# Performance work log

Hardware: AMD Instinct MI355X
Metric: run time of the kernel (lower is better)

The kernel has to match this reference:

```python
import jax, jax.numpy as jnp
import numpy as np

FACTOR = 2.0
SCALE = 0.2
SOFTMAX_N = 0.0  # softmax_n param; n=0 -> standard softmax

B, H, S, D = 2, 16, 2048, 64


def setup_inputs() -> dict:
    key = jax.random.key(0)
    kq, kk, kv = jax.random.split(key, 3)
    return {
        "query": jax.random.normal(kq, (B, H, S, D), dtype=jnp.float32),
        "key": jax.random.normal(kk, (B, H, S, D), dtype=jnp.float32),
        "value": jax.random.normal(kv, (B, H, S, D), dtype=jnp.float32),
    }


def softmax_n(x, n):
    # exp(x) / (n + sum(exp(x))), numerically stable.
    m = jnp.max(x, axis=-1, keepdims=True)
    e = jnp.exp(x - m)
    denom = n * jnp.exp(-m) + jnp.sum(e, axis=-1, keepdims=True)
    return e / denom


def reference(query, key, value):
    # scores: [B,H,S,S]
    scores = jnp.einsum("bhqd,bhkd->bhqk", query, key) * SCALE
    attn = softmax_n(scores, SOFTMAX_N)
    out = jnp.einsum("bhqk,bhkd->bhqd", attn, value)
    return FACTOR * out
```

## Files before the change

### kernel.cpp

```cpp
#include <hip/hip_runtime.h>
#include <stdint.h>

typedef __attribute__((ext_vector_type(4))) float f32x4;
typedef __attribute__((ext_vector_type(8))) short s16x8;

__device__ __forceinline__ short f2bf(float f) {
    union { float f; uint32_t u; } v; v.f = f;
    uint32_t r = (v.u + 0x7FFFu + ((v.u >> 16) & 1u)) >> 16;
    return (short)(uint16_t)r;
}

__device__ __forceinline__ void async16(const short* g, short* lds) {
  __builtin_amdgcn_global_load_lds(
      (const __attribute__((address_space(1))) uint32_t*)g,
      (__attribute__((address_space(3))) uint32_t*)lds, 16, 0, 0);
}

__global__ __launch_bounds__(256) void conv_k_kernel(const float* __restrict__ K,
                                                     short* __restrict__ Kbf) {
  const int i = (blockIdx.x * 256 + threadIdx.x) * 8;
  f32x4 a = *(const f32x4*)(K + i);
  f32x4 b = *(const f32x4*)(K + i + 4);
  union { short s[8]; int4 v; } p;
#pragma unroll
  for (int j = 0; j < 4; ++j) { p.s[j] = f2bf(a[j]); p.s[4 + j] = f2bf(b[j]); }
  *(int4*)(Kbf + i) = p.v;
}

__global__ __launch_bounds__(256) void conv_vt_kernel(const float* __restrict__ V,
                                                      short* __restrict__ VT) {
  __shared__ short t[64][72];
  const int bh = blockIdx.x >> 5;
  const int st = blockIdx.x & 31;
  const size_t base = (size_t)bh * 131072;
  {
    const int s_loc = threadIdx.x >> 2;
    const int dch = (threadIdx.x & 3) * 16;
    const float* p = V + base + (size_t)(st * 64 + s_loc) * 64 + dch;
#pragma unroll
    for (int j = 0; j < 16; j += 4) {
      f32x4 a = *(const f32x4*)(p + j);
#pragma unroll
      for (int q = 0; q < 4; ++q) t[s_loc][dch + j + q] = f2bf(a[q]);
    }
  }
  __syncthreads();
  {
    const int d_loc = threadIdx.x >> 2;
    const int sch = (threadIdx.x & 3) * 16;
    union { short s[16]; int4 v[2]; } o;
#pragma unroll
    for (int j = 0; j < 16; ++j) o.s[j] = t[sch + j][d_loc];
    short* out = VT + base + (size_t)d_loc * 2048 + st * 64 + sch;
    *(int4*)(out) = o.v[0];
    *(int4*)(out + 8) = o.v[1];
  }
}

__global__ __launch_bounds__(256) void attn_fwd_v2(
    const float* __restrict__ Q, const short* __restrict__ Kbf,
    const short* __restrict__ VT, float* __restrict__ O) {
  constexpr int S = 2048, D = 64;
  constexpr float SCALE = 0.2f, FACTOR = 2.0f;
  constexpr int NT = S / 64;

  __shared__ short kT[2][4096];
  __shared__ short vT[2][4096];
  __shared__ short pT[4][1024];

  const int tid = threadIdx.x;
  const int w = tid >> 6;
  const int l = tid & 63;
  const int g = l >> 4;
  const int c = l & 15;

  const int rid = (blockIdx.x & 7) * 128 + (blockIdx.x >> 3);
  const int bh = rid >> 5;
  const int qt = rid & 31;
  const size_t base = (size_t)bh * (size_t)(S * D);

  const short* Kp = Kbf + base;
  const short* Vp = VT + base;
  char* pB = (char*)pT[w];

  s16x8 qa[2];
  {
    const float* qp = Q + base + (size_t)(qt * 64 + w * 16 + c) * D + g * 8;
#pragma unroll
    for (int kk = 0; kk < 2; ++kk) {
      f32x4 q0 = *(const f32x4*)(qp + kk * 32);
      f32x4 q1 = *(const f32x4*)(qp + kk * 32 + 4);
      s16x8 a;
#pragma unroll
      for (int i = 0; i < 4; ++i) { a[i] = f2bf(q0[i]); a[4 + i] = f2bf(q1[i]); }
      qa[kk] = a;
    }
  }

  int kOff[2], vOff[2], ldsT[2];
#pragma unroll
  for (int i = 0; i < 2; ++i) {
    const int t = i * 256 + w * 64 + l;
    const int row = t >> 3, ch = t & 7;
    ldsT[i] = t * 8;
    kOff[i] = row * 64 + ((ch ^ (row & 7)) << 3);
    vOff[i] = row * 2048 + ((ch ^ (row & 7)) << 3);
  }
#define STAGE(buf, kv0s)                                        \
  do {                                                          \
    _Pragma("unroll") for (int i = 0; i < 2; ++i) {             \
      async16(Kp + (kv0s) * 64 + kOff[i], &kT[buf][ldsT[i]]);   \
      async16(Vp + (kv0s) + vOff[i], &vT[buf][ldsT[i]]);        \
    }                                                           \
  } while (0)

  f32x4 o_acc[4];
#pragma unroll
  for (int nb = 0; nb < 4; ++nb) o_acc[nb] = (f32x4){0.f, 0.f, 0.f, 0.f};
  float m_r[4], l_r[4];
#pragma unroll
  for (int r = 0; r < 4; ++r) { m_r[r] = -1e30f; l_r[r] = 0.f; }

  int cur = 0;
  STAGE(0, 0);
  for (int kt = 0; kt < NT; ++kt) {
    __syncthreads();
    if (kt + 1 < NT) STAGE(cur ^ 1, (kt + 1) * 64);

    const char* kB = (const char*)kT[cur];
    const char* vB = (const char*)vT[cur];

    f32x4 sc[4];
#pragma unroll
    for (int nb = 0; nb < 4; ++nb) sc[nb] = (f32x4){0.f, 0.f, 0.f, 0.f};
#pragma unroll
    for (int kk = 0; kk < 2; ++kk) {
#pragma unroll
      for (int nb = 0; nb < 4; ++nb) {
        const int row = nb * 16 + c;
        s16x8 b = *(const s16x8*)(kB + row * 128 +
                                  ((kk * 64 + g * 16) ^ ((row & 7) << 4)));
        sc[nb] = __builtin_amdgcn_mfma_f32_16x16x32_bf16(qa[kk], b, sc[nb], 0, 0, 0);
      }
    }

    float p[4][4];
    float esc[4];
#pragma unroll
    for (int r = 0; r < 4; ++r) {
      float mx = fmaxf(fmaxf(sc[0][r], sc[1][r]), fmaxf(sc[2][r], sc[3][r]));
#pragma unroll
      for (int mask = 1; mask < 16; mask <<= 1)
        mx = fmaxf(mx, __shfl_xor(mx, mask, 64));
      mx *= SCALE;
      const float mnew = fmaxf(m_r[r], mx);
      esc[r] = __expf(m_r[r] - mnew);
      float rs = 0.f;
#pragma unroll
      for (int nb = 0; nb < 4; ++nb) {
        float e = __expf(sc[nb][r] * SCALE - mnew);
        p[nb][r] = e;
        rs += e;
      }
#pragma unroll
      for (int mask = 1; mask < 16; mask <<= 1)
        rs += __shfl_xor(rs, mask, 64);
      l_r[r] = l_r[r] * esc[r] + rs;
      m_r[r] = mnew;
    }
#pragma unroll
    for (int nb = 0; nb < 4; ++nb)
#pragma unroll
      for (int r = 0; r < 4; ++r)
        o_acc[nb][r] *= esc[r];

#pragma unroll
    for (int nb = 0; nb < 4; ++nb) {
#pragma unroll
      for (int r = 0; r < 4; ++r) {
        const int row = 4 * g + r;
        const int colb = (nb * 16 + c) * 2;
        *(short*)(pB + row * 128 + (colb ^ ((row & 7) << 4))) = f2bf(p[nb][r]);
      }
    }
    asm volatile("s_waitcnt lgkmcnt(0)" ::: "memory");

#pragma unroll
    for (int kk = 0; kk < 2; ++kk) {
      s16x8 pa = *(const s16x8*)(pB + c * 128 +
                                 ((kk * 64 + g * 16) ^ ((c & 7) << 4)));
#pragma unroll
      for (int nb = 0; nb < 4; ++nb) {
        const int row = nb * 16 + c;
        s16x8 vb = *(const s16x8*)(vB + row * 128 +
                                   ((kk * 64 + g * 16) ^ ((row & 7) << 4)));
        o_acc[nb] = __builtin_amdgcn_mfma_f32_16x16x32_bf16(pa, vb, o_acc[nb], 0, 0, 0);
      }
    }
    cur ^= 1;
  }
#undef STAGE

#pragma unroll
  for (int r = 0; r < 4; ++r) {
    const float f = FACTOR / l_r[r];
    const size_t rowg = (size_t)(qt * 64 + w * 16 + 4 * g + r);
    float* op = O + base + rowg * D + c;
#pragma unroll
    for (int nb = 0; nb < 4; ++nb) op[nb * 16] = o_acc[nb][r] * f;
  }
}

__global__ __launch_bounds__(256) void attn_fwd_v1(
    const float* __restrict__ Q, const float* __restrict__ K,
    const float* __restrict__ V, float* __restrict__ O) {
  constexpr int S = 2048, D = 64;
  constexpr float SCALE = 0.2f, FACTOR = 2.0f;
  constexpr int KVBLK = 64, NT = S / KVBLK;
  __shared__ short kT[64 * 64];
  __shared__ short vT[64 * 64];
  __shared__ short pT[4][16 * 64];
  const int tid = threadIdx.x;
  const int w = tid >> 6, l = tid & 63, g = l >> 4, c = l & 15;
  const int bh = blockIdx.x >> 5, qt = blockIdx.x & 31;
  const size_t base = (size_t)bh * (size_t)(S * D);
  char* kB = (char*)kT; char* vB = (char*)vT; char* pB = (char*)pT[w];
  s16x8 qa[2];
  {
    const float* qp = Q + base + (size_t)(qt * 64 + w * 16 + c) * D + g * 8;
#pragma unroll
    for (int kk = 0; kk < 2; ++kk) {
      f32x4 q0 = *(const f32x4*)(qp + kk * 32);
      f32x4 q1 = *(const f32x4*)(qp + kk * 32 + 4);
      s16x8 a;
#pragma unroll
      for (int i = 0; i < 4; ++i) { a[i] = f2bf(q0[i]); a[4 + i] = f2bf(q1[i]); }
      qa[kk] = a;
    }
  }
  f32x4 o_acc[4];
#pragma unroll
  for (int nb = 0; nb < 4; ++nb) o_acc[nb] = (f32x4){0.f, 0.f, 0.f, 0.f};
  float m_r[4], l_r[4];
#pragma unroll
  for (int r = 0; r < 4; ++r) { m_r[r] = -1e30f; l_r[r] = 0.f; }
  const int krow = tid >> 2, kcb = tid & 3;
  const int vpr = (tid >> 3) * 2, vpc = (tid & 7) * 8;
  for (int kt = 0; kt < NT; ++kt) {
    const int kv0 = kt * KVBLK;
    __syncthreads();
    {
      const float* kp = K + base + (size_t)(kv0 + krow) * D + kcb * 16;
      f32x4 a0 = *(const f32x4*)(kp);
      f32x4 a1 = *(const f32x4*)(kp + 4);
      f32x4 a2 = *(const f32x4*)(kp + 8);
      f32x4 a3 = *(const f32x4*)(kp + 12);
      union { short s[8]; int4 v; } p0, p1;
#pragma unroll
      for (int i = 0; i < 4; ++i) {
        p0.s[i] = f2bf(a0[i]); p0.s[4 + i] = f2bf(a1[i]);
        p1.s[i] = f2bf(a2[i]); p1.s[4 + i] = f2bf(a3[i]);
      }
      const int sw = (krow & 7) << 4;
      *(int4*)(kB + krow * 128 + ((kcb * 32) ^ sw)) = p0.v;
      *(int4*)(kB + krow * 128 + ((kcb * 32 + 16) ^ sw)) = p1.v;
    }
    {
      const float* vp = V + base + (size_t)(kv0 + vpr) * D + vpc;
      f32x4 r0a = *(const f32x4*)(vp);
      f32x4 r0b = *(const f32x4*)(vp + 4);
      f32x4 r1a = *(const f32x4*)(vp + D);
      f32x4 r1b = *(const f32x4*)(vp + D + 4);
      float lo[8] = {r0a[0], r0a[1], r0a[2], r0a[3], r0b[0], r0b[1], r0b[2], r0b[3]};
      float hi[8] = {r1a[0], r1a[1], r1a[2], r1a[3], r1b[0], r1b[1], r1b[2], r1b[3]};
#pragma unroll
      for (int i = 0; i < 8; ++i) {
        uint32_t pk = (uint32_t)(uint16_t)f2bf(lo[i]) |
                      ((uint32_t)(uint16_t)f2bf(hi[i]) << 16);
        const int col = vpc + i;
        *(uint32_t*)(vB + col * 128 + ((vpr * 2) ^ ((col & 7) << 4))) = pk;
      }
    }
    __syncthreads();
    f32x4 sc[4];
#pragma unroll
    for (int nb = 0; nb < 4; ++nb) sc[nb] = (f32x4){0.f, 0.f, 0.f, 0.f};
#pragma unroll
    for (int kk = 0; kk < 2; ++kk) {
#pragma unroll
      for (int nb = 0; nb < 4; ++nb) {
        const int row = nb * 16 + c;
        s16x8 b = *(const s16x8*)(kB + row * 128 +
                                  ((kk * 64 + g * 16) ^ ((row & 7) << 4)));
        sc[nb] = __builtin_amdgcn_mfma_f32_16x16x32_bf16(qa[kk], b, sc[nb], 0, 0, 0);
      }
    }
    float p[4][4]; float esc[4];
#pragma unroll
    for (int r = 0; r < 4; ++r) {
      float mx = fmaxf(fmaxf(sc[0][r], sc[1][r]), fmaxf(sc[2][r], sc[3][r]));
#pragma unroll
      for (int mask = 1; mask < 16; mask <<= 1)
        mx = fmaxf(mx, __shfl_xor(mx, mask, 64));
      mx *= SCALE;
      const float mnew = fmaxf(m_r[r], mx);
      esc[r] = __expf(m_r[r] - mnew);
      float rs = 0.f;
#pragma unroll
      for (int nb = 0; nb < 4; ++nb) {
        float e = __expf(sc[nb][r] * SCALE - mnew);
        p[nb][r] = e; rs += e;
      }
#pragma unroll
      for (int mask = 1; mask < 16; mask <<= 1)
        rs += __shfl_xor(rs, mask, 64);
      l_r[r] = l_r[r] * esc[r] + rs;
      m_r[r] = mnew;
    }
#pragma unroll
    for (int nb = 0; nb < 4; ++nb)
#pragma unroll
      for (int r = 0; r < 4; ++r) o_acc[nb][r] *= esc[r];
#pragma unroll
    for (int nb = 0; nb < 4; ++nb) {
#pragma unroll
      for (int r = 0; r < 4; ++r) {
        const int row = 4 * g + r;
        const int colb = (nb * 16 + c) * 2;
        *(short*)(pB + row * 128 + (colb ^ ((row & 7) << 4))) = f2bf(p[nb][r]);
      }
    }
    asm volatile("s_waitcnt lgkmcnt(0)" ::: "memory");
#pragma unroll
    for (int kk = 0; kk < 2; ++kk) {
      s16x8 pa = *(const s16x8*)(pB + c * 128 +
                                 ((kk * 64 + g * 16) ^ ((c & 7) << 4)));
#pragma unroll
      for (int nb = 0; nb < 4; ++nb) {
        const int row = nb * 16 + c;
        s16x8 vb = *(const s16x8*)(vB + row * 128 +
                                   ((kk * 64 + g * 16) ^ ((row & 7) << 4)));
        o_acc[nb] = __builtin_amdgcn_mfma_f32_16x16x32_bf16(pa, vb, o_acc[nb], 0, 0, 0);
      }
    }
  }
#pragma unroll
  for (int r = 0; r < 4; ++r) {
    const float f = FACTOR / l_r[r];
    const size_t rowg = (size_t)(qt * 64 + w * 16 + 4 * g + r);
    float* op = O + base + rowg * D + c;
#pragma unroll
    for (int nb = 0; nb < 4; ++nb) op[nb * 16] = o_acc[nb][r] * f;
  }
}

extern "C" void kernel_launch(void* const* d_in, const int* in_sizes, int n_in,
                              void* d_out, int out_size, void* d_ws, size_t ws_size,
                              hipStream_t stream) {
  (void)in_sizes; (void)n_in; (void)out_size;
  const float* Q = (const float*)d_in[0];
  const float* K = (const float*)d_in[1];
  const float* V = (const float*)d_in[2];
  float* O = (float*)d_out;
  constexpr size_t NEED = 2ull * 2 * 16 * 2048 * 64 * sizeof(short);
  if (ws_size >= NEED && d_ws) {
    short* Kbf = (short*)d_ws;
    short* VT = Kbf + 2 * 16 * 2048 * 64;
    hipLaunchKernelGGL(conv_k_kernel, dim3(2048), dim3(256), 0, stream, K, Kbf);
    hipLaunchKernelGGL(conv_vt_kernel, dim3(1024), dim3(256), 0, stream, V, VT);
    hipLaunchKernelGGL(attn_fwd_v2, dim3(1024), dim3(256), 0, stream, Q, Kbf, VT, O);
  } else {
    hipLaunchKernelGGL(attn_fwd_v1, dim3(1024), dim3(256), 0, stream, Q, K, V, O);
  }
}
```

Before: 201.5 us.

## Rewrite attention with 32x32 MFMA, register-resident P, exp2 softmax and lazy rescale

Replaces the attention kernel with a version that computes S^T using 32x32x16 bf16 MFMAs, so each lane holds a column of probabilities. This lets P be packed straight into MFMA operands with no LDS round-trip. Scale and log2e are folded into Q so the softmax uses exp2. The running max is only rescaled when the new max exceeds a threshold, and s_setprio is set around the MFMA blocks. Each block now covers 128 query rows (512 blocks), and the K conversion and V transpose are merged into one prep kernel. The risks are fewer blocks, higher register pressure, and possible precision loss from the lazy rescale.

```diff
diff --git a/kernel.cpp b/kernel.cpp
--- a/kernel.cpp
+++ b/kernel.cpp
@@ -1,7 +1,9 @@
 #include <hip/hip_runtime.h>
+#include <hip/hip_bf16.h>
 #include <stdint.h>
 
 typedef __attribute__((ext_vector_type(4))) float f32x4;
+typedef __attribute__((ext_vector_type(16))) float f32x16;
 typedef __attribute__((ext_vector_type(8))) short s16x8;
 
 __device__ __forceinline__ short f2bf(float f) {
@@ -10,29 +12,42 @@
     return (short)(uint16_t)r;
 }
 
+__device__ __forceinline__ uint32_t pk2(float a, float b) {
+  union { __hip_bfloat162 h; uint32_t u; } v;
+  v.h = __float22bfloat162_rn(make_float2(a, b));
+  return v.u;
+}
+
 __device__ __forceinline__ void async16(const short* g, short* lds) {
   __builtin_amdgcn_global_load_lds(
       (const __attribute__((address_space(1))) uint32_t*)g,
       (__attribute__((address_space(3))) uint32_t*)lds, 16, 0, 0);
 }
 
-__global__ __launch_bounds__(256) void conv_k_kernel(const float* __restrict__ K,
-                                                     short* __restrict__ Kbf) {
-  const int i = (blockIdx.x * 256 + threadIdx.x) * 8;
-  f32x4 a = *(const f32x4*)(K + i);
-  f32x4 b = *(const f32x4*)(K + i + 4);
-  union { short s[8]; int4 v; } p;
-#pragma unroll
-  for (int j = 0; j < 4; ++j) { p.s[j] = f2bf(a[j]); p.s[4 + j] = f2bf(b[j]); }
-  *(int4*)(Kbf + i) = p.v;
-}
-
-__global__ __launch_bounds__(256) void conv_vt_kernel(const float* __restrict__ V,
-                                                      short* __restrict__ VT) {
+__global__ __launch_bounds__(256) void conv_kv_kernel(
+    const float* __restrict__ K, const float* __restrict__ V,
+    short* __restrict__ Kbf, short* __restrict__ VT) {
   __shared__ short t[64][72];
   const int bh = blockIdx.x >> 5;
   const int st = blockIdx.x & 31;
   const size_t base = (size_t)bh * 131072;
+
+  {
+    const int row = threadIdx.x >> 2;
+    const int cb = (threadIdx.x & 3) * 16;
+    const float* kp = K + base + (size_t)(st * 64 + row) * 64 + cb;
+    union { short s[16]; int4 v[2]; } o;
+#pragma unroll
+    for (int j = 0; j < 16; j += 4) {
+      f32x4 a = *(const f32x4*)(kp + j);
+#pragma unroll
+      for (int q = 0; q < 4; ++q) o.s[j + q] = f2bf(a[q]);
+    }
+    short* out = Kbf + base + (size_t)(st * 64 + row) * 64 + cb;
+    *(int4*)(out) = o.v[0];
+    *(int4*)(out + 8) = o.v[1];
+  }
+
   {
     const int s_loc = threadIdx.x >> 2;
     const int dch = (threadIdx.x & 3) * 16;
@@ -50,164 +65,172 @@
     const int sch = (threadIdx.x & 3) * 16;
     union { short s[16]; int4 v[2]; } o;
 #pragma unroll
-    for (int j = 0; j < 16; ++j) o.s[j] = t[sch + j][d_loc];
+    for (int i = 0; i < 4; ++i) {
+      o.s[i]      = t[sch + i][d_loc];
+      o.s[4 + i]  = t[sch + 8 + i][d_loc];
+      o.s[8 + i]  = t[sch + 4 + i][d_loc];
+      o.s[12 + i] = t[sch + 12 + i][d_loc];
+    }
     short* out = VT + base + (size_t)d_loc * 2048 + st * 64 + sch;
     *(int4*)(out) = o.v[0];
     *(int4*)(out + 8) = o.v[1];
   }
 }
 
-__global__ __launch_bounds__(256) void attn_fwd_v2(
+__global__ __launch_bounds__(256) void attn_fwd_v3(
     const float* __restrict__ Q, const short* __restrict__ Kbf,
     const short* __restrict__ VT, float* __restrict__ O) {
   constexpr int S = 2048, D = 64;
-  constexpr float SCALE = 0.2f, FACTOR = 2.0f;
   constexpr int NT = S / 64;
+  constexpr float K1 = 0.28853901f;
+  constexpr float THR = 11.5415603f;
 
   __shared__ short kT[2][4096];
-  __shared__ short vT[2][4096];
-  __shared__ short pT[4][1024];
+  __shared__ short vS[2][4096];
 
   const int tid = threadIdx.x;
   const int w = tid >> 6;
   const int l = tid & 63;
-  const int g = l >> 4;
-  const int c = l & 15;
-
-  const int rid = (blockIdx.x & 7) * 128 + (blockIdx.x >> 3);
-  const int bh = rid >> 5;
-  const int qt = rid & 31;
+  const int hi = l >> 5;
+  const int c32 = l & 31;
+
+  const int rid = (blockIdx.x & 7) * 64 + (blockIdx.x >> 3);
+  const int bh = rid >> 4;
+  const int qt = rid & 15;
   const size_t base = (size_t)bh * (size_t)(S * D);
+  const int qrow = qt * 128 + w * 32 + c32;
 
   const short* Kp = Kbf + base;
   const short* Vp = VT + base;
-  char* pB = (char*)pT[w];
-
-  s16x8 qa[2];
-  {
-    const float* qp = Q + base + (size_t)(qt * 64 + w * 16 + c) * D + g * 8;
-#pragma unroll
-    for (int kk = 0; kk < 2; ++kk) {
-      f32x4 q0 = *(const f32x4*)(qp + kk * 32);
-      f32x4 q1 = *(const f32x4*)(qp + kk * 32 + 4);
-      s16x8 a;
-#pragma unroll
-      for (int i = 0; i < 4; ++i) { a[i] = f2bf(q0[i]); a[4 + i] = f2bf(q1[i]); }
-      qa[kk] = a;
-    }
-  }
-
-  int kOff[2], vOff[2], ldsT[2];
+
+  s16x8 qreg[4];
+  {
+    const float* qp = Q + base + (size_t)qrow * D;
+#pragma unroll
+    for (int j = 0; j < 4; ++j) {
+      f32x4 a = *(const f32x4*)(qp + j * 16 + hi * 8);
+      f32x4 b = *(const f32x4*)(qp + j * 16 + hi * 8 + 4);
+      union { uint32_t u[4]; s16x8 v; } pk;
+      pk.u[0] = pk2(a[0] * K1, a[1] * K1);
+      pk.u[1] = pk2(a[2] * K1, a[3] * K1);
+      pk.u[2] = pk2(b[0] * K1, b[1] * K1);
+      pk.u[3] = pk2(b[2] * K1, b[3] * K1);
+      qreg[j] = pk.v;
+    }
+  }
+
+  int kSrc[2], vSrc[2], ldsOff[2];
 #pragma unroll
   for (int i = 0; i < 2; ++i) {
-    const int t = i * 256 + w * 64 + l;
+    const int t = i * 256 + tid;
     const int row = t >> 3, ch = t & 7;
-    ldsT[i] = t * 8;
-    kOff[i] = row * 64 + ((ch ^ (row & 7)) << 3);
-    vOff[i] = row * 2048 + ((ch ^ (row & 7)) << 3);
-  }
-#define STAGE(buf, kv0s)                                        \
-  do {                                                          \
-    _Pragma("unroll") for (int i = 0; i < 2; ++i) {             \
-      async16(Kp + (kv0s) * 64 + kOff[i], &kT[buf][ldsT[i]]);   \
-      async16(Vp + (kv0s) + vOff[i], &vT[buf][ldsT[i]]);        \
-    }                                                           \
+    ldsOff[i] = t * 8;
+    kSrc[i] = row * 64 + ((ch ^ (row & 7)) << 3);
+    vSrc[i] = row * 2048 + ((ch ^ (row & 7)) << 3);
+  }
+#define STAGE(buf, kv0)                                       \
+  do {                                                        \
+    _Pragma("unroll") for (int i = 0; i < 2; ++i) {           \
+      async16(Kp + (kv0) * 64 + kSrc[i], &kT[buf][ldsOff[i]]); \
+      async16(Vp + (kv0) + vSrc[i], &vS[buf][ldsOff[i]]);      \
+    }                                                         \
   } while (0)
 
-  f32x4 o_acc[4];
-#pragma unroll
-  for (int nb = 0; nb < 4; ++nb) o_acc[nb] = (f32x4){0.f, 0.f, 0.f, 0.f};
-  float m_r[4], l_r[4];
-#pragma unroll
-  for (int r = 0; r < 4; ++r) { m_r[r] = -1e30f; l_r[r] = 0.f; }
+  f32x16 o0, o1;
+#pragma unroll
+  for (int i = 0; i < 16; ++i) { o0[i] = 0.f; o1[i] = 0.f; }
+  float m = -1e30f, lsum = 0.f;
 
   int cur = 0;
   STAGE(0, 0);
   for (int kt = 0; kt < NT; ++kt) {
     __syncthreads();
     if (kt + 1 < NT) STAGE(cur ^ 1, (kt + 1) * 64);
-
     const char* kB = (const char*)kT[cur];
-    const char* vB = (const char*)vT[cur];
-
-    f32x4 sc[4];
-#pragma unroll
-    for (int nb = 0; nb < 4; ++nb) sc[nb] = (f32x4){0.f, 0.f, 0.f, 0.f};
-#pragma unroll
-    for (int kk = 0; kk < 2; ++kk) {
-#pragma unroll
-      for (int nb = 0; nb < 4; ++nb) {
-        const int row = nb * 16 + c;
-        s16x8 b = *(const s16x8*)(kB + row * 128 +
-                                  ((kk * 64 + g * 16) ^ ((row & 7) << 4)));
-        sc[nb] = __builtin_amdgcn_mfma_f32_16x16x32_bf16(qa[kk], b, sc[nb], 0, 0, 0);
-      }
-    }
-
-    float p[4][4];
-    float esc[4];
-#pragma unroll
-    for (int r = 0; r < 4; ++r) {
-      float mx = fmaxf(fmaxf(sc[0][r], sc[1][r]), fmaxf(sc[2][r], sc[3][r]));
-#pragma unroll
-      for (int mask = 1; mask < 16; mask <<= 1)
-        mx = fmaxf(mx, __shfl_xor(mx, mask, 64));
-      mx *= SCALE;
-      const float mnew = fmaxf(m_r[r], mx);
-      esc[r] = __expf(m_r[r] - mnew);
-      float rs = 0.f;
-#pragma unroll
-      for (int nb = 0; nb < 4; ++nb) {
-        float e = __expf(sc[nb][r] * SCALE - mnew);
-        p[nb][r] = e;
-        rs += e;
-      }
-#pragma unroll
-      for (int mask = 1; mask < 16; mask <<= 1)
-        rs += __shfl_xor(rs, mask, 64);
-      l_r[r] = l_r[r] * esc[r] + rs;
-      m_r[r] = mnew;
-    }
-#pragma unroll
-    for (int nb = 0; nb < 4; ++nb)
-#pragma unroll
-      for (int r = 0; r < 4; ++r)
-        o_acc[nb][r] *= esc[r];
-
-#pragma unroll
-    for (int nb = 0; nb < 4; ++nb) {
-#pragma unroll
-      for (int r = 0; r < 4; ++r) {
-        const int row = 4 * g + r;
-        const int colb = (nb * 16 + c) * 2;
-        *(short*)(pB + row * 128 + (colb ^ ((row & 7) << 4))) = f2bf(p[nb][r]);
-      }
-    }
-    asm volatile("s_waitcnt lgkmcnt(0)" ::: "memory");
-
-#pragma unroll
-    for (int kk = 0; kk < 2; ++kk) {
-      s16x8 pa = *(const s16x8*)(pB + c * 128 +
-                                 ((kk * 64 + g * 16) ^ ((c & 7) << 4)));
-#pragma unroll
-      for (int nb = 0; nb < 4; ++nb) {
-        const int row = nb * 16 + c;
-        s16x8 vb = *(const s16x8*)(vB + row * 128 +
-                                   ((kk * 64 + g * 16) ^ ((row & 7) << 4)));
-        o_acc[nb] = __builtin_amdgcn_mfma_f32_16x16x32_bf16(pa, vb, o_acc[nb], 0, 0, 0);
-      }
+    const char* vB = (const char*)vS[cur];
+
+#pragma unroll
+    for (int grp = 0; grp < 2; ++grp) {
+      f32x16 s;
+#pragma unroll
+      for (int i = 0; i < 16; ++i) s[i] = 0.f;
+      const int krow = grp * 32 + c32;
+      const int ksw = (krow & 7) << 4;
+      __builtin_amdgcn_s_setprio(1);
+#pragma unroll
+      for (int j = 0; j < 4; ++j) {
+        s16x8 a = *(const s16x8*)(kB + krow * 128 + ((j * 32 + hi * 16) ^ ksw));
+        s = __builtin_amdgcn_mfma_f32_32x32x16_bf16(a, qreg[j], s, 0, 0, 0);
+      }
+      __builtin_amdgcn_s_setprio(0);
+
+      float t8[8];
+#pragma unroll
+      for (int i = 0; i < 8; ++i) t8[i] = fmaxf(s[2 * i], s[2 * i + 1]);
+      float t4a = fmaxf(fmaxf(t8[0], t8[1]), fmaxf(t8[2], t8[3]));
+      float t4b = fmaxf(fmaxf(t8[4], t8[5]), fmaxf(t8[6], t8[7]));
+      float tm = fmaxf(t4a, t4b);
+      tm = fmaxf(tm, __shfl_xor(tm, 32));
+      if (!__all(tm <= m + THR)) {
+        const float mn = fmaxf(m, tm);
+        const float scl = exp2f(m - mn);
+        lsum *= scl;
+        o0 *= scl;
+        o1 *= scl;
+        m = mn;
+      }
+      float p[16];
+#pragma unroll
+      for (int i = 0; i < 16; ++i) p[i] = exp2f(s[i] - m);
+      float s8[8];
+#pragma unroll
+      for (int i = 0; i < 8; ++i) s8[i] = p[2 * i] + p[2 * i + 1];
+      float rsa = (s8[0] + s8[1]) + (s8[2] + s8[3]);
+      float rsb = (s8[4] + s8[5]) + (s8[6] + s8[7]);
+      float rs = rsa + rsb;
+      rs += __shfl_xor(rs, 32);
+      lsum += rs;
+
+      union { uint32_t u[8]; s16x8 v[2]; } wp;
+#pragma unroll
+      for (int i = 0; i < 8; ++i) wp.u[i] = pk2(p[2 * i], p[2 * i + 1]);
+
+      __builtin_amdgcn_s_setprio(1);
+#pragma unroll
+      for (int c = 0; c < 2; ++c) {
+        const s16x8 bp = wp.v[c];
+        {
+          const int vrow = c32;
+          s16x8 av = *(const s16x8*)(vB + vrow * 128 +
+                                     ((grp * 64 + c * 32 + hi * 16) ^ ((vrow & 7) << 4)));
+          o0 = __builtin_amdgcn_mfma_f32_32x32x16_bf16(av, bp, o0, 0, 0, 0);
+        }
+        {
+          const int vrow = 32 + c32;
+          s16x8 av = *(const s16x8*)(vB + vrow * 128 +
+                                     ((grp * 64 + c * 32 + hi * 16) ^ ((vrow & 7) << 4)));
+          o1 = __builtin_amdgcn_mfma_f32_32x32x16_bf16(av, bp, o1, 0, 0, 0);
+        }
+      }
+      __builtin_amdgcn_s_setprio(0);
     }
     cur ^= 1;
   }
 #undef STAGE
 
-#pragma unroll
-  for (int r = 0; r < 4; ++r) {
-    const float f = FACTOR / l_r[r];
-    const size_t rowg = (size_t)(qt * 64 + w * 16 + 4 * g + r);
-    float* op = O + base + rowg * D + c;
-#pragma unroll
-    for (int nb = 0; nb < 4; ++nb) op[nb * 16] = o_acc[nb][r] * f;
+  const float f = 2.0f / lsum;
+  float* op = O + base + (size_t)qrow * D;
+#pragma unroll
+  for (int rq = 0; rq < 4; ++rq) {
+    const int d0 = rq * 8 + 4 * hi;
+    f32x4 v0, v1;
+#pragma unroll
+    for (int i = 0; i < 4; ++i) {
+      v0[i] = o0[rq * 4 + i] * f;
+      v1[i] = o1[rq * 4 + i] * f;
+    }
+    *(f32x4*)(op + d0) = v0;
+    *(f32x4*)(op + d0 + 32) = v1;
   }
 }
 
@@ -272,11 +295,11 @@
       f32x4 r1a = *(const f32x4*)(vp + D);
       f32x4 r1b = *(const f32x4*)(vp + D + 4);
       float lo[8] = {r0a[0], r0a[1], r0a[2], r0a[3], r0b[0], r0b[1], r0b[2], r0b[3]};
-      float hi[8] = {r1a[0], r1a[1], r1a[2], r1a[3], r1b[0], r1b[1], r1b[2], r1b[3]};
+      float hi2[8] = {r1a[0], r1a[1], r1a[2], r1a[3], r1b[0], r1b[1], r1b[2], r1b[3]};
 #pragma unroll
       for (int i = 0; i < 8; ++i) {
         uint32_t pk = (uint32_t)(uint16_t)f2bf(lo[i]) |
-                      ((uint32_t)(uint16_t)f2bf(hi[i]) << 16);
+                      ((uint32_t)(uint16_t)f2bf(hi2[i]) << 16);
         const int col = vpc + i;
         *(uint32_t*)(vB + col * 128 + ((vpr * 2) ^ ((col & 7) << 4))) = pk;
       }
@@ -366,9 +389,8 @@
   if (ws_size >= NEED && d_ws) {
     short* Kbf = (short*)d_ws;
     short* VT = Kbf + 2 * 16 * 2048 * 64;
-    hipLaunchKernelGGL(conv_k_kernel, dim3(2048), dim3(256), 0, stream, K, Kbf);
-    hipLaunchKernelGGL(conv_vt_kernel, dim3(1024), dim3(256), 0, stream, V, VT);
-    hipLaunchKernelGGL(attn_fwd_v2, dim3(1024), dim3(256), 0, stream, Q, Kbf, VT, O);
+    hipLaunchKernelGGL(conv_kv_kernel, dim3(1024), dim3(256), 0, stream, K, V, Kbf, VT);
+    hipLaunchKernelGGL(attn_fwd_v3, dim3(512), dim3(256), 0, stream, Q, Kbf, VT, O);
   } else {
     hipLaunchKernelGGL(attn_fwd_v1, dim3(1024), dim3(256), 0, stream, Q, K, V, O);
   }
```

Result: faster. 169.5 us (-15.9%).
